# Kernel tuning notes

Hardware: AMD Instinct MI355X
Metric: run time of the kernel (lower is better)

The kernel has to match this reference:

```python
import jax, jax.numpy as jnp
import numpy as np

B, V = 4, 5                      # batch_size, nview
CUBE = (80, 80, 20)              # PICT_STRUCT.CUBE_SIZE
NBINS = CUBE[0] * CUBE[1] * CUBE[2]
IMG_W, IMG_H = 960, 512          # NETWORK.IMAGE_SIZE (w, h)
ORI_W, ORI_H = 1920, 1080        # NETWORK.ORI_IMAGE_SIZE
HM_W, HM_H = 240, 128            # NETWORK.HEATMAP_SIZE
C_IMG, C_FEAT = 3, 32
C_TOT = C_IMG + C_FEAT
HID = 256
D_IN = 3 + 2 * C_TOT             # points + [mean, var] volume features


def setup_inputs():
    key = jax.random.key(0)
    ks = jax.random.split(key, 10)
    denorm_imgs = jax.random.uniform(ks[0], (V, B, C_IMG, IMG_H, IMG_W), jnp.float32)
    feats2d = jax.random.normal(ks[1], (V, B, C_FEAT, HM_H, HM_W), jnp.float32)
    lo = jnp.array([-1500.0, -1500.0, -300.0], jnp.float32)
    hi = jnp.array([1500.0, 1500.0, 300.0], jnp.float32)
    grids = lo + (hi - lo) * jax.random.uniform(ks[2], (B, NBINS, 3), jnp.float32)
    # near-identity rotations, camera centers ~3m behind the volume so all
    # points project inside the original image
    R = jnp.tile(jnp.eye(3, dtype=jnp.float32), (V, B, 1, 1)) \
        + 0.01 * jax.random.normal(ks[3], (V, B, 3, 3), jnp.float32)
    T = jnp.tile(jnp.array([0.0, 0.0, -3000.0], jnp.float32).reshape(3, 1), (V, B, 1, 1)) \
        + 50.0 * jax.random.normal(ks[4], (V, B, 3, 1), jnp.float32)
    f = 1500.0 + 10.0 * jax.random.normal(ks[5], (V, B, 2), jnp.float32)
    c_cam = jnp.tile(jnp.array([ORI_W / 2.0, ORI_H / 2.0], jnp.float32), (V, B, 1))
    k_dist = jnp.zeros((V, B, 3), jnp.float32)
    p_dist = jnp.zeros((V, B, 2), jnp.float32)
    resize_transform = jnp.array([[IMG_W / ORI_W, 0.0, 0.0],
                                  [0.0, IMG_H / ORI_H, 0.0]], jnp.float32)
    s1, s2 = 1.0 / np.sqrt(D_IN), 1.0 / np.sqrt(HID)
    W1 = (s1 * jax.random.normal(ks[6], (D_IN, HID))).astype(jnp.float32)
    b1 = jnp.zeros((HID,), jnp.float32)
    W2 = (s2 * jax.random.normal(ks[7], (HID, HID))).astype(jnp.float32)
    b2 = jnp.zeros((HID,), jnp.float32)
    W3 = (s2 * jax.random.normal(ks[8], (HID, 1))).astype(jnp.float32)
    b3 = jnp.zeros((1,), jnp.float32)
    return dict(denorm_imgs=denorm_imgs, feats2d=feats2d, grids=grids, R=R, T=T,
                f=f, c_cam=c_cam, k_dist=k_dist, p_dist=p_dist,
                resize_transform=resize_transform,
                W1=W1, b1=b1, W2=W2, b2=b2, W3=W3, b3=b3)


def _project(x, R, T, f, c, k, p):
    # voxelpose project_point_radial: x [N,3] world-mm -> [N,2] pixel coords
    xcam = R @ (x.T - T)                               # [3,N]
    y = xcam[:2] / (xcam[2:3] + 1e-5)                  # [2,N]
    r2 = jnp.sum(y * y, axis=0)
    radial = 1.0 + k[0] * r2 + k[1] * r2 ** 2 + k[2] * r2 ** 3
    tan = p[0] * y[1] + p[1] * y[0]
    y = y * (radial + 2.0 * tan)[None, :] + jnp.stack([p[1], p[0]])[:, None] * r2[None, :]
    return (f[:, None] * y + c[:, None]).T             # [N,2]


def _bilinear(img, gx, gy):
    # F.grid_sample bilinear, align_corners=True, padding_mode='zeros'
    # img: [C,H,W]; gx,gy: [N] in [-1,1] -> [C,N]
    C, H, W = img.shape
    x = (gx + 1.0) * 0.5 * (W - 1)
    y = (gy + 1.0) * 0.5 * (H - 1)
    x0, y0 = jnp.floor(x), jnp.floor(y)
    wx1, wy1 = x - x0, y - y0
    wx0, wy0 = 1.0 - wx1, 1.0 - wy1

    def tap(xi, yi):
        valid = (xi >= 0) & (xi <= W - 1) & (yi >= 0) & (yi <= H - 1)
        xi_c = jnp.clip(xi.astype(jnp.int32), 0, W - 1)
        yi_c = jnp.clip(yi.astype(jnp.int32), 0, H - 1)
        return img[:, yi_c, xi_c] * valid.astype(img.dtype)

    return (tap(x0, y0) * (wx0 * wy0) + tap(x0 + 1.0, y0) * (wx1 * wy0)
            + tap(x0, y0 + 1.0) * (wx0 * wy1) + tap(x0 + 1.0, y0 + 1.0) * (wx1 * wy1))


def _sample_view(img, feat, pts, R, T, f, c, k, p, trans):
    xy = _project(pts, R, T, f, c, k, p)
    xy = jnp.clip(xy, -1.0, float(max(ORI_W, ORI_H)))
    xy = jnp.concatenate([xy, jnp.ones((xy.shape[0], 1), xy.dtype)], axis=1) @ trans.T
    g = xy / jnp.array([IMG_W - 1.0, IMG_H - 1.0], jnp.float32) * 2.0 - 1.0
    si = _bilinear(img, g[:, 0], g[:, 1])              # [C_IMG, N]
    sf = _bilinear(feat, g[:, 0], g[:, 1])             # [C_FEAT, N]
    return jnp.concatenate([si, sf], axis=0)           # [C_TOT, N]


def reference(denorm_imgs, feats2d, grids, R, T, f, c_cam, k_dist, p_dist,
              resize_transform, W1, b1, W2, b2, W3, b3):
    per_b = jax.vmap(_sample_view, in_axes=(0, 0, 0, 0, 0, 0, 0, 0, 0, None))
    per_vb = jax.vmap(per_b, in_axes=(0, 0, None, 0, 0, 0, 0, 0, 0, None))
    cubes = per_vb(denorm_imgs, feats2d, grids, R, T, f, c_cam, k_dist, p_dist,
                   resize_transform)                   # [V,B,C,N]
    cubes = jnp.transpose(cubes, (1, 2, 3, 0))         # [B,C,N,V]
    mean = jnp.mean(cubes, axis=-1)                    # sum(cubes/nview)
    var = jnp.sum((cubes - mean[..., None]) ** 2, axis=-1) / V
    var = jnp.exp(-var)
    gvol = jnp.concatenate([mean, var], axis=1)        # [B,2C,N]
    # nerf_model.query_density: MLP over (points, per-point global volume feats)
    feat = jnp.concatenate([grids / 1000.0, jnp.swapaxes(gvol, 1, 2)], axis=-1)  # [B,N,D_IN]
    h = jax.nn.relu(feat @ W1 + b1)
    h = jax.nn.relu(h @ W2 + b2)
    density = jax.nn.softplus(h @ W3 + b3)             # [B,N,1]
    alpha = 1.0 - jnp.exp(-density)
    return alpha.reshape(B, 1, CUBE[0], CUBE[1], CUBE[2])
```

## Files before the change

### kernel.cpp

```cpp
#include <hip/hip_runtime.h>

#define NVIEW 5
#define BATCH 4
#define NPTS 128000
#define CIMG 3
#define CFEAT 32
#define CTOT 35
#define DIN 73
#define HID 256
#define IMG_W 960
#define IMG_H 512
#define HM_W 240
#define HM_H 128
#define HW_IMG (IMG_W * IMG_H)
#define HW_HM (HM_W * HM_H)

#define BP 32

#define NB_IMG  (NVIEW * BATCH * HW_IMG / 4 / 256)
#define NB_FEAT (NVIEW * BATCH * HW_HM / 256)
#define NB_W    44

typedef __attribute__((ext_vector_type(8))) short bf16x8;
typedef __attribute__((ext_vector_type(4))) float f32x4;
typedef __attribute__((ext_vector_type(4))) unsigned short ushort4v;
typedef __attribute__((ext_vector_type(8))) unsigned short ushort8v;

__device__ inline unsigned short bf16_rtne(float f) {
    unsigned u = __builtin_bit_cast(unsigned, f);
    u += 0x7FFFu + ((u >> 16) & 1u);
    return (unsigned short)(u >> 16);
}
__device__ inline float bf2f(unsigned short u) {
    return __builtin_bit_cast(float, ((unsigned)u) << 16);
}

struct Tap {
    int o00, o01, o10, o11;
    float w00, w01, w10, w11;
};

__device__ inline void make_tap(float gx, float gy, int W, int H, Tap& t) {
    float x = (gx + 1.0f) * 0.5f * (float)(W - 1);
    float y = (gy + 1.0f) * 0.5f * (float)(H - 1);
    float x0 = floorf(x), y0 = floorf(y);
    float x1 = x0 + 1.0f, y1 = y0 + 1.0f;
    float wx1 = x - x0, wy1 = y - y0;
    float wx0 = 1.0f - wx1, wy0 = 1.0f - wy1;
    float vx0 = (x0 >= 0.0f && x0 <= (float)(W - 1)) ? 1.0f : 0.0f;
    float vx1 = (x1 >= 0.0f && x1 <= (float)(W - 1)) ? 1.0f : 0.0f;
    float vy0 = (y0 >= 0.0f && y0 <= (float)(H - 1)) ? 1.0f : 0.0f;
    float vy1 = (y1 >= 0.0f && y1 <= (float)(H - 1)) ? 1.0f : 0.0f;
    int ix0 = min(max((int)x0, 0), W - 1);
    int ix1 = min(max((int)x1, 0), W - 1);
    int iy0 = min(max((int)y0, 0), H - 1);
    int iy1 = min(max((int)y1, 0), H - 1);
    t.o00 = iy0 * W + ix0;  t.w00 = wx0 * wy0 * vx0 * vy0;
    t.o01 = iy0 * W + ix1;  t.w01 = wx1 * wy0 * vx1 * vy0;
    t.o10 = iy1 * W + ix0;  t.w10 = wx0 * wy1 * vx0 * vy1;
    t.o11 = iy1 * W + ix1;  t.w11 = wx1 * wy1 * vx1 * vy1;
}

__device__ inline float4 f4zero() { float4 r; r.x = r.y = r.z = r.w = 0.f; return r; }
__device__ inline float4 tapacc(ushort4v a, float w, float4 acc) {
    acc.x += w * bf2f(a[0]); acc.y += w * bf2f(a[1]);
    acc.z += w * bf2f(a[2]); acc.w += w * bf2f(a[3]); return acc;
}
__device__ inline float4 f4add(float4 a, float4 b) {
    a.x += b.x; a.y += b.y; a.z += b.z; a.w += b.w; return a;
}
__device__ inline float4 f4addsq(float4 acc, float4 v) {
    acc.x += v.x * v.x; acc.y += v.y * v.y; acc.z += v.z * v.z; acc.w += v.w * v.w; return acc;
}

__global__ __launch_bounds__(256) void prep_all(const float* __restrict__ imgs,
                                                const float* __restrict__ feats,
                                                const float* __restrict__ W1,
                                                const float* __restrict__ W2,
                                                unsigned short* __restrict__ wsImg,
                                                unsigned short* __restrict__ wsFeat,
                                                unsigned short* __restrict__ W1b,
                                                unsigned short* __restrict__ W2b) {
    int blk = blockIdx.x;
    if (blk < NB_IMG) {
        int idx = blk * 256 + threadIdx.x;
        int vb = idx / (HW_IMG / 4);
        int p4 = idx - vb * (HW_IMG / 4);
        const float* src = imgs + (size_t)vb * 3 * HW_IMG + p4 * 4;
        float4 c0 = *reinterpret_cast<const float4*>(src);
        float4 c1 = *reinterpret_cast<const float4*>(src + HW_IMG);
        float4 c2 = *reinterpret_cast<const float4*>(src + 2 * HW_IMG);
        ushort8v o01, o23;
        o01[0] = bf16_rtne(c0.x); o01[1] = bf16_rtne(c1.x); o01[2] = bf16_rtne(c2.x); o01[3] = 0;
        o01[4] = bf16_rtne(c0.y); o01[5] = bf16_rtne(c1.y); o01[6] = bf16_rtne(c2.y); o01[7] = 0;
        o23[0] = bf16_rtne(c0.z); o23[1] = bf16_rtne(c1.z); o23[2] = bf16_rtne(c2.z); o23[3] = 0;
        o23[4] = bf16_rtne(c0.w); o23[5] = bf16_rtne(c1.w); o23[6] = bf16_rtne(c2.w); o23[7] = 0;
        ushort8v* dst = reinterpret_cast<ushort8v*>(wsImg + ((size_t)vb * HW_IMG + p4 * 4) * 4);
        dst[0] = o01;
        dst[1] = o23;
    } else if (blk < NB_IMG + NB_FEAT) {
        int idx = (blk - NB_IMG) * 256 + threadIdx.x;
        int vb = idx / HW_HM;
        int pix = idx - vb * HW_HM;
        const float* src = feats + (size_t)vb * 32 * HW_HM + pix;
        ushort8v* dst = reinterpret_cast<ushort8v*>(wsFeat + (size_t)idx * 32);
#pragma unroll
        for (int k = 0; k < 4; ++k) {
            ushort8v o;
#pragma unroll
            for (int j = 0; j < 8; ++j)
                o[j] = bf16_rtne(src[(8 * k + j) * HW_HM]);
            dst[k] = o;
        }
    } else {
        int idx = (blk - NB_IMG - NB_FEAT) * 256 + threadIdx.x;
        if (idx < 16 * 3 * 64) {
            int l = idx & 63;
            int ks = (idx >> 6) % 3;
            int nt = idx / 192;
            int n = nt * 16 + (l & 15);
            int k0 = ks * 32 + (l >> 4) * 8;
            ushort8v o;
#pragma unroll
            for (int j = 0; j < 8; ++j) {
                int k = k0 + j;
                float v = (k < DIN) ? W1[k * HID + n] : 0.0f;
                o[j] = bf16_rtne(v);
            }
            reinterpret_cast<ushort8v*>(W1b)[idx] = o;
        } else if (idx < 16 * 3 * 64 + 16 * 8 * 64) {
            int id2 = idx - 16 * 3 * 64;
            int l = id2 & 63;
            int ks = (id2 >> 6) & 7;
            int nt = id2 >> 9;
            int n = nt * 16 + (l & 15);
            int k0 = ks * 32 + (l >> 4) * 8;
            ushort8v o;
#pragma unroll
            for (int j = 0; j < 8; ++j)
                o[j] = bf16_rtne(W2[(k0 + j) * HID + n]);
            reinterpret_cast<ushort8v*>(W2b)[id2] = o;
        }
    }
}

__global__ __launch_bounds__(256, 6) void fused_denorm_project(
    const unsigned short* __restrict__ wsImg,
    const unsigned short* __restrict__ wsFeat,
    const unsigned short* __restrict__ W1b,
    const unsigned short* __restrict__ W2b,
    const float* __restrict__ grids,
    const float* __restrict__ Rm,
    const float* __restrict__ Tm,
    const float* __restrict__ fcam,
    const float* __restrict__ ccam,
    const float* __restrict__ kdist,
    const float* __restrict__ pdist,
    const float* __restrict__ trans,
    const float* __restrict__ b1,
    const float* __restrict__ b2,
    const float* __restrict__ W3,
    const float* __restrict__ b3,
    float* __restrict__ out)
{
    __shared__ unsigned short featb[BP * 96];
    __shared__ unsigned short h1T[BP * 256];
    __shared__ float b1L[HID], b2L[HID], w3L[HID];
    __shared__ float partial[4][BP];

    const int tid = threadIdx.x;
    const int blk = blockIdx.x;
    const int b   = blk / (NPTS / BP);
    const int n0  = (blk % (NPTS / BP)) * BP;

    b1L[tid] = b1[tid];
    b2L[tid] = b2[tid];
    w3L[tid] = W3[tid];

    {
        const int t = tid & 7;
        const int p = tid >> 3;
        const int n = n0 + p;
        char* fbB = (char*)featb;
        const int rowoff = p * 192;
        const int sw = (p & 7) << 4;

        const float px = grids[(b * NPTS + n) * 3 + 0];
        const float py = grids[(b * NPTS + n) * 3 + 1];
        const float pz = grids[(b * NPTS + n) * 3 + 2];
        if (t == 1) {
            *(unsigned short*)(fbB + ((rowoff + 0) ^ sw)) = bf16_rtne(px * 1e-3f);
            *(unsigned short*)(fbB + ((rowoff + 2) ^ sw)) = bf16_rtne(py * 1e-3f);
            *(unsigned short*)(fbB + ((rowoff + 4) ^ sw)) = bf16_rtne(pz * 1e-3f);
        }
        {
            int c0 = 73 + t * 3;
            int cnt = (t == 7) ? 2 : 3;
            for (int j = 0; j < cnt; ++j)
                *(unsigned short*)(fbB + ((rowoff + (c0 + j) * 2) ^ sw)) = 0;
        }

        Tap myF = {}; Tap myI = {};
        if (t < NVIEW) {
            const int vb = t * BATCH + b;
            const float* Rp = Rm + vb * 9;
            const float* Tp = Tm + vb * 3;
            float X = px - Tp[0], Y = py - Tp[1], Z = pz - Tp[2];
            float xc = Rp[0] * X + Rp[1] * Y + Rp[2] * Z;
            float yc = Rp[3] * X + Rp[4] * Y + Rp[5] * Z;
            float zc = Rp[6] * X + Rp[7] * Y + Rp[8] * Z;
            float inv = 1.0f / (zc + 1e-5f);
            float y0 = xc * inv, y1 = yc * inv;
            float r2 = y0 * y0 + y1 * y1;
            float k0 = kdist[vb * 3 + 0], k1 = kdist[vb * 3 + 1], k2 = kdist[vb * 3 + 2];
            float p0 = pdist[vb * 2 + 0], p1 = pdist[vb * 2 + 1];
            float radial = 1.0f + r2 * (k0 + r2 * (k1 + r2 * k2));
            float tn = p0 * y1 + p1 * y0;
            float scl = radial + 2.0f * tn;
            float uu = y0 * scl + p1 * r2;
            float vv = y1 * scl + p0 * r2;
            float xo = fcam[vb * 2 + 0] * uu + ccam[vb * 2 + 0];
            float yo = fcam[vb * 2 + 1] * vv + ccam[vb * 2 + 1];
            xo = fminf(fmaxf(xo, -1.0f), 1920.0f);
            yo = fminf(fmaxf(yo, -1.0f), 1920.0f);
            float xr = trans[0] * xo + trans[1] * yo + trans[2];
            float yr = trans[3] * xo + trans[4] * yo + trans[5];
            float gx = xr * (1.0f / (float)(IMG_W - 1)) * 2.0f - 1.0f;
            float gy = yr * (1.0f / (float)(IMG_H - 1)) * 2.0f - 1.0f;
            make_tap(gx, gy, HM_W, HM_H, myF);
            make_tap(gx, gy, IMG_W, IMG_H, myI);
        }

        float4 s4 = f4zero(), q4 = f4zero();
        const int lb = (tid & 63) & 56;
        for (int v = 0; v < NVIEW; ++v) {
            const int src = lb + v;
            Tap tF;
            tF.o00 = __shfl(myF.o00, src, 64);
            tF.o01 = __shfl(myF.o01, src, 64);
            tF.o10 = __shfl(myF.o10, src, 64);
            tF.o11 = __shfl(myF.o11, src, 64);
            tF.w00 = __shfl(myF.w00, src, 64);
            tF.w01 = __shfl(myF.w01, src, 64);
            tF.w10 = __shfl(myF.w10, src, 64);
            tF.w11 = __shfl(myF.w11, src, 64);
            const unsigned short* fb = wsFeat + (size_t)(v * BATCH + b) * HW_HM * 32 + t * 4;
            ushort4v a00 = *reinterpret_cast<const ushort4v*>(fb + (size_t)tF.o00 * 32);
            ushort4v a01 = *reinterpret_cast<const ushort4v*>(fb + (size_t)tF.o01 * 32);
            ushort4v a10 = *reinterpret_cast<const ushort4v*>(fb + (size_t)tF.o10 * 32);
            ushort4v a11 = *reinterpret_cast<const ushort4v*>(fb + (size_t)tF.o11 * 32);
            float4 val = f4zero();
            val = tapacc(a00, tF.w00, val);
            val = tapacc(a01, tF.w01, val);
            val = tapacc(a10, tF.w10, val);
            val = tapacc(a11, tF.w11, val);
            s4 = f4add(s4, val);
            q4 = f4addsq(q4, val);
        }

        float4 si = f4zero(), qi = f4zero();
        if (t < NVIEW) {
            const unsigned short* ib = wsImg + (size_t)(t * BATCH + b) * HW_IMG * 4;
            ushort4v i00 = *reinterpret_cast<const ushort4v*>(ib + (size_t)myI.o00 * 4);
            ushort4v i01 = *reinterpret_cast<const ushort4v*>(ib + (size_t)myI.o01 * 4);
            ushort4v i10 = *reinterpret_cast<const ushort4v*>(ib + (size_t)myI.o10 * 4);
            ushort4v i11 = *reinterpret_cast<const ushort4v*>(ib + (size_t)myI.o11 * 4);
            float4 vi = f4zero();
            vi = tapacc(i00, myI.w00, vi);
            vi = tapacc(i01, myI.w01, vi);
            vi = tapacc(i10, myI.w10, vi);
            vi = tapacc(i11, myI.w11, vi);
            si = vi;
            qi = f4addsq(f4zero(), vi);
        }
#pragma unroll
        for (int off = 1; off <= 4; off <<= 1) {
            si.x += __shfl_xor(si.x, off, 64);
            si.y += __shfl_xor(si.y, off, 64);
            si.z += __shfl_xor(si.z, off, 64);
            qi.x += __shfl_xor(qi.x, off, 64);
            qi.y += __shfl_xor(qi.y, off, 64);
            qi.z += __shfl_xor(qi.z, off, 64);
        }

        const float inv5 = 1.0f / (float)NVIEW;
        {
            float m0 = s4.x * inv5, m1 = s4.y * inv5, m2 = s4.z * inv5, m3 = s4.w * inv5;
            int cm = 6 + 4 * t;
            int cv = 41 + 4 * t;
            *(unsigned short*)(fbB + ((rowoff + (cm + 0) * 2) ^ sw)) = bf16_rtne(m0);
            *(unsigned short*)(fbB + ((rowoff + (cm + 1) * 2) ^ sw)) = bf16_rtne(m1);
            *(unsigned short*)(fbB + ((rowoff + (cm + 2) * 2) ^ sw)) = bf16_rtne(m2);
            *(unsigned short*)(fbB + ((rowoff + (cm + 3) * 2) ^ sw)) = bf16_rtne(m3);
            *(unsigned short*)(fbB + ((rowoff + (cv + 0) * 2) ^ sw)) = bf16_rtne(expf(-(q4.x * inv5 - m0 * m0)));
            *(unsigned short*)(fbB + ((rowoff + (cv + 1) * 2) ^ sw)) = bf16_rtne(expf(-(q4.y * inv5 - m1 * m1)));
            *(unsigned short*)(fbB + ((rowoff + (cv + 2) * 2) ^ sw)) = bf16_rtne(expf(-(q4.z * inv5 - m2 * m2)));
            *(unsigned short*)(fbB + ((rowoff + (cv + 3) * 2) ^ sw)) = bf16_rtne(expf(-(q4.w * inv5 - m3 * m3)));
        }
        if (t == 0) {
            float m0 = si.x * inv5, m1 = si.y * inv5, m2 = si.z * inv5;
            *(unsigned short*)(fbB + ((rowoff + 3 * 2) ^ sw)) = bf16_rtne(m0);
            *(unsigned short*)(fbB + ((rowoff + 4 * 2) ^ sw)) = bf16_rtne(m1);
            *(unsigned short*)(fbB + ((rowoff + 5 * 2) ^ sw)) = bf16_rtne(m2);
            *(unsigned short*)(fbB + ((rowoff + 38 * 2) ^ sw)) = bf16_rtne(expf(-(qi.x * inv5 - m0 * m0)));
            *(unsigned short*)(fbB + ((rowoff + 39 * 2) ^ sw)) = bf16_rtne(expf(-(qi.y * inv5 - m1 * m1)));
            *(unsigned short*)(fbB + ((rowoff + 40 * 2) ^ sw)) = bf16_rtne(expf(-(qi.z * inv5 - m2 * m2)));
        }
    }
    __syncthreads();

    const int l   = tid & 63;
    const int w   = tid >> 6;
    const int g   = l >> 4;
    const int c16 = l & 15;

    {
        f32x4 acc[4][2];
#pragma unroll
        for (int nl = 0; nl < 4; ++nl)
#pragma unroll
            for (int pt = 0; pt < 2; ++pt) acc[nl][pt] = (f32x4)0.0f;

        const bf16x8* wfrag = reinterpret_cast<const bf16x8*>(W1b);
#pragma unroll
        for (int ks = 0; ks < 3; ++ks) {
            bf16x8 bfr[2];
#pragma unroll
            for (int pt = 0; pt < 2; ++pt) {
                int p = pt * 16 + c16;
                int off = (p * 192 + (ks * 32 + g * 8) * 2) ^ ((p & 7) << 4);
                bfr[pt] = *reinterpret_cast<const bf16x8*>((const char*)featb + off);
            }
#pragma unroll
            for (int nl = 0; nl < 4; ++nl) {
                int nt = w * 4 + nl;
                bf16x8 a = wfrag[(nt * 3 + ks) * 64 + l];
                acc[nl][0] = __builtin_amdgcn_mfma_f32_16x16x32_bf16(a, bfr[0], acc[nl][0], 0, 0, 0);
                acc[nl][1] = __builtin_amdgcn_mfma_f32_16x16x32_bf16(a, bfr[1], acc[nl][1], 0, 0, 0);
            }
        }
#pragma unroll
        for (int nl = 0; nl < 4; ++nl) {
            int nb = (w * 4 + nl) * 16 + g * 4;
            float bb0 = b1L[nb + 0], bb1 = b1L[nb + 1], bb2 = b1L[nb + 2], bb3v = b1L[nb + 3];
#pragma unroll
            for (int pt = 0; pt < 2; ++pt) {
                int p = pt * 16 + c16;
                ushort4v pk;
                pk[0] = bf16_rtne(fmaxf(acc[nl][pt][0] + bb0, 0.0f));
                pk[1] = bf16_rtne(fmaxf(acc[nl][pt][1] + bb1, 0.0f));
                pk[2] = bf16_rtne(fmaxf(acc[nl][pt][2] + bb2, 0.0f));
                pk[3] = bf16_rtne(fmaxf(acc[nl][pt][3] + bb3v, 0.0f));
                int off = (p * 512 + nb * 2) ^ ((p & 7) << 4);
                *reinterpret_cast<ushort4v*>((char*)h1T + off) = pk;
            }
        }
    }
    __syncthreads();

    {
        f32x4 acc[4][2];
#pragma unroll
        for (int nl = 0; nl < 4; ++nl)
#pragma unroll
            for (int pt = 0; pt < 2; ++pt) acc[nl][pt] = (f32x4)0.0f;

        const bf16x8* wfrag = reinterpret_cast<const bf16x8*>(W2b);
#pragma unroll
        for (int ks = 0; ks < 8; ++ks) {
            bf16x8 bfr[2];
#pragma unroll
            for (int pt = 0; pt < 2; ++pt) {
                int p = pt * 16 + c16;
                int off = (p * 512 + (ks * 32 + g * 8) * 2) ^ ((p & 7) << 4);
                bfr[pt] = *reinterpret_cast<const bf16x8*>((const char*)h1T + off);
            }
#pragma unroll
            for (int nl = 0; nl < 4; ++nl) {
                int nt = w * 4 + nl;
                bf16x8 a = wfrag[(nt * 8 + ks) * 64 + l];
                acc[nl][0] = __builtin_amdgcn_mfma_f32_16x16x32_bf16(a, bfr[0], acc[nl][0], 0, 0, 0);
                acc[nl][1] = __builtin_amdgcn_mfma_f32_16x16x32_bf16(a, bfr[1], acc[nl][1], 0, 0, 0);
            }
        }
        float s0 = 0.0f, s1 = 0.0f;
#pragma unroll
        for (int nl = 0; nl < 4; ++nl) {
            int nb = (w * 4 + nl) * 16 + g * 4;
#pragma unroll
            for (int r = 0; r < 4; ++r) {
                float b2v = b2L[nb + r];
                float w3v = w3L[nb + r];
                s0 += fmaxf(acc[nl][0][r] + b2v, 0.0f) * w3v;
                s1 += fmaxf(acc[nl][1][r] + b2v, 0.0f) * w3v;
            }
        }
        s0 += __shfl_xor(s0, 16, 64);
        s0 += __shfl_xor(s0, 32, 64);
        s1 += __shfl_xor(s1, 16, 64);
        s1 += __shfl_xor(s1, 32, 64);
        if (g == 0) {
            partial[w][c16]      = s0;
            partial[w][16 + c16] = s1;
        }
    }
    __syncthreads();

    if (tid < BP) {
        float v = partial[0][tid] + partial[1][tid] + partial[2][tid] + partial[3][tid] + b3[0];
        out[b * NPTS + n0 + tid] = 1.0f / (1.0f + expf(-v));
    }
}

extern "C" void kernel_launch(void* const* d_in, const int* in_sizes, int n_in,
                              void* d_out, int out_size, void* d_ws, size_t ws_size,
                              hipStream_t stream) {
    const float* imgs  = (const float*)d_in[0];
    const float* feats = (const float*)d_in[1];
    const float* grids = (const float*)d_in[2];
    const float* Rm    = (const float*)d_in[3];
    const float* Tm    = (const float*)d_in[4];
    const float* fcam  = (const float*)d_in[5];
    const float* ccam  = (const float*)d_in[6];
    const float* kdist = (const float*)d_in[7];
    const float* pdist = (const float*)d_in[8];
    const float* trans = (const float*)d_in[9];
    const float* W1    = (const float*)d_in[10];
    const float* b1    = (const float*)d_in[11];
    const float* W2    = (const float*)d_in[12];
    const float* b2    = (const float*)d_in[13];
    const float* W3    = (const float*)d_in[14];
    const float* b3    = (const float*)d_in[15];
    float* out = (float*)d_out;

    unsigned short* wsImg  = (unsigned short*)d_ws;
    unsigned short* wsFeat = wsImg + (size_t)NVIEW * BATCH * HW_IMG * 4;
    unsigned short* W1b    = wsFeat + (size_t)NVIEW * BATCH * HW_HM * 32;
    unsigned short* W2b    = W1b + 16 * 3 * 64 * 8;

    prep_all<<<NB_IMG + NB_FEAT + NB_W, 256, 0, stream>>>(
        imgs, feats, W1, W2, wsImg, wsFeat, W1b, W2b);

    const int nblocks = BATCH * (NPTS / BP);
    fused_denorm_project<<<nblocks, 256, 0, stream>>>(
        wsImg, wsFeat, W1b, W2b, grids, Rm, Tm, fcam, ccam, kdist, pdist, trans,
        b1, b2, W3, b3, out);
}
```

Measured before the change: 490.4 us.

## Merge prep and main kernels into one persistent kernel with grid barrier

Replaces the separate bf16 conversion kernel and the per-tile MLP kernel with a single persistent kernel of fixed grid size. Each block first runs grid-stride conversion of images, features and weights, then all blocks meet at an atomic-counter grid barrier, then each block loops over point tiles. This removes one kernel launch and the gap between the two kernels, and lets blocks stay resident across tiles. It adds a memset per call and relies on all 1536 blocks being co-resident, otherwise the spin barrier deadlocks. It also drops the tail overlap the launch boundary previously allowed.

```diff
diff --git a/kernel.cpp b/kernel.cpp
--- a/kernel.cpp
+++ b/kernel.cpp
@@ -16,10 +16,8 @@
 #define HW_HM (HM_W * HM_H)
 
 #define BP 32
-
-#define NB_IMG  (NVIEW * BATCH * HW_IMG / 4 / 256)
-#define NB_FEAT (NVIEW * BATCH * HW_HM / 256)
-#define NB_W    44
+#define TILES (BATCH * (NPTS / BP))
+#define GRID 1536
 
 typedef __attribute__((ext_vector_type(8))) short bf16x8;
 typedef __attribute__((ext_vector_type(4))) float f32x4;
@@ -73,19 +71,35 @@
     acc.x += v.x * v.x; acc.y += v.y * v.y; acc.z += v.z * v.z; acc.w += v.w * v.w; return acc;
 }
 
-__global__ __launch_bounds__(256) void prep_all(const float* __restrict__ imgs,
-                                                const float* __restrict__ feats,
-                                                const float* __restrict__ W1,
-                                                const float* __restrict__ W2,
-                                                unsigned short* __restrict__ wsImg,
-                                                unsigned short* __restrict__ wsFeat,
-                                                unsigned short* __restrict__ W1b,
-                                                unsigned short* __restrict__ W2b) {
-    int blk = blockIdx.x;
-    if (blk < NB_IMG) {
-        int idx = blk * 256 + threadIdx.x;
-        int vb = idx / (HW_IMG / 4);
-        int p4 = idx - vb * (HW_IMG / 4);
+__global__ __launch_bounds__(256, 6) void fused_all(
+    const float* __restrict__ imgs,
+    const float* __restrict__ feats,
+    const float* __restrict__ grids,
+    const float* __restrict__ Rm, const float* __restrict__ Tm,
+    const float* __restrict__ fcam, const float* __restrict__ ccam,
+    const float* __restrict__ kdist, const float* __restrict__ pdist,
+    const float* __restrict__ trans,
+    const float* __restrict__ W1, const float* __restrict__ b1,
+    const float* __restrict__ W2, const float* __restrict__ b2,
+    const float* __restrict__ W3, const float* __restrict__ b3,
+    unsigned short* __restrict__ wsImg,
+    unsigned short* __restrict__ wsFeat,
+    unsigned short* __restrict__ W1b,
+    unsigned short* __restrict__ W2b,
+    unsigned* __restrict__ ctr,
+    float* __restrict__ out)
+{
+    __shared__ unsigned short featb[BP * 96];
+    __shared__ unsigned short h1T[BP * 256];
+    __shared__ float b1L[HID], b2L[HID], w3L[HID];
+    __shared__ float partial[4][BP];
+
+    const int tid = threadIdx.x;
+    const unsigned gtid = blockIdx.x * 256u + (unsigned)tid;
+
+    for (unsigned u = gtid; u < (unsigned)(NVIEW * BATCH) * (HW_IMG / 4); u += GRID * 256u) {
+        unsigned vb = u / (HW_IMG / 4);
+        unsigned p4 = u - vb * (HW_IMG / 4);
         const float* src = imgs + (size_t)vb * 3 * HW_IMG + p4 * 4;
         float4 c0 = *reinterpret_cast<const float4*>(src);
         float4 c1 = *reinterpret_cast<const float4*>(src + HW_IMG);
@@ -98,12 +112,12 @@
         ushort8v* dst = reinterpret_cast<ushort8v*>(wsImg + ((size_t)vb * HW_IMG + p4 * 4) * 4);
         dst[0] = o01;
         dst[1] = o23;
-    } else if (blk < NB_IMG + NB_FEAT) {
-        int idx = (blk - NB_IMG) * 256 + threadIdx.x;
-        int vb = idx / HW_HM;
-        int pix = idx - vb * HW_HM;
+    }
+    for (unsigned u = gtid; u < (unsigned)(NVIEW * BATCH) * HW_HM; u += GRID * 256u) {
+        unsigned vb = u / HW_HM;
+        unsigned pix = u - vb * HW_HM;
         const float* src = feats + (size_t)vb * 32 * HW_HM + pix;
-        ushort8v* dst = reinterpret_cast<ushort8v*>(wsFeat + (size_t)idx * 32);
+        ushort8v* dst = reinterpret_cast<ushort8v*>(wsFeat + (size_t)u * 32);
 #pragma unroll
         for (int k = 0; k < 4; ++k) {
             ushort8v o;
@@ -112,303 +126,289 @@
                 o[j] = bf16_rtne(src[(8 * k + j) * HW_HM]);
             dst[k] = o;
         }
-    } else {
-        int idx = (blk - NB_IMG - NB_FEAT) * 256 + threadIdx.x;
-        if (idx < 16 * 3 * 64) {
-            int l = idx & 63;
-            int ks = (idx >> 6) % 3;
-            int nt = idx / 192;
-            int n = nt * 16 + (l & 15);
-            int k0 = ks * 32 + (l >> 4) * 8;
-            ushort8v o;
-#pragma unroll
-            for (int j = 0; j < 8; ++j) {
-                int k = k0 + j;
-                float v = (k < DIN) ? W1[k * HID + n] : 0.0f;
-                o[j] = bf16_rtne(v);
-            }
-            reinterpret_cast<ushort8v*>(W1b)[idx] = o;
-        } else if (idx < 16 * 3 * 64 + 16 * 8 * 64) {
-            int id2 = idx - 16 * 3 * 64;
-            int l = id2 & 63;
-            int ks = (id2 >> 6) & 7;
-            int nt = id2 >> 9;
-            int n = nt * 16 + (l & 15);
-            int k0 = ks * 32 + (l >> 4) * 8;
-            ushort8v o;
-#pragma unroll
-            for (int j = 0; j < 8; ++j)
-                o[j] = bf16_rtne(W2[(k0 + j) * HID + n]);
-            reinterpret_cast<ushort8v*>(W2b)[id2] = o;
-        }
     }
-}
-
-__global__ __launch_bounds__(256, 6) void fused_denorm_project(
-    const unsigned short* __restrict__ wsImg,
-    const unsigned short* __restrict__ wsFeat,
-    const unsigned short* __restrict__ W1b,
-    const unsigned short* __restrict__ W2b,
-    const float* __restrict__ grids,
-    const float* __restrict__ Rm,
-    const float* __restrict__ Tm,
-    const float* __restrict__ fcam,
-    const float* __restrict__ ccam,
-    const float* __restrict__ kdist,
-    const float* __restrict__ pdist,
-    const float* __restrict__ trans,
-    const float* __restrict__ b1,
-    const float* __restrict__ b2,
-    const float* __restrict__ W3,
-    const float* __restrict__ b3,
-    float* __restrict__ out)
-{
-    __shared__ unsigned short featb[BP * 96];
-    __shared__ unsigned short h1T[BP * 256];
-    __shared__ float b1L[HID], b2L[HID], w3L[HID];
-    __shared__ float partial[4][BP];
-
-    const int tid = threadIdx.x;
-    const int blk = blockIdx.x;
-    const int b   = blk / (NPTS / BP);
-    const int n0  = (blk % (NPTS / BP)) * BP;
+    if (gtid < 16 * 3 * 64) {
+        int idx = (int)gtid;
+        int l = idx & 63;
+        int ks = (idx >> 6) % 3;
+        int nt = idx / 192;
+        int n = nt * 16 + (l & 15);
+        int k0 = ks * 32 + (l >> 4) * 8;
+        ushort8v o;
+#pragma unroll
+        for (int j = 0; j < 8; ++j) {
+            int k = k0 + j;
+            float v = (k < DIN) ? W1[k * HID + n] : 0.0f;
+            o[j] = bf16_rtne(v);
+        }
+        reinterpret_cast<ushort8v*>(W1b)[idx] = o;
+    } else if (gtid < 16 * 3 * 64 + 16 * 8 * 64) {
+        int id2 = (int)gtid - 16 * 3 * 64;
+        int l = id2 & 63;
+        int ks = (id2 >> 6) & 7;
+        int nt = id2 >> 9;
+        int n = nt * 16 + (l & 15);
+        int k0 = ks * 32 + (l >> 4) * 8;
+        ushort8v o;
+#pragma unroll
+        for (int j = 0; j < 8; ++j)
+            o[j] = bf16_rtne(W2[(k0 + j) * HID + n]);
+        reinterpret_cast<ushort8v*>(W2b)[id2] = o;
+    }
+
+    __syncthreads();
+    if (tid == 0) {
+        __hip_atomic_fetch_add(ctr, 1u, __ATOMIC_RELEASE, __HIP_MEMORY_SCOPE_AGENT);
+        while (__hip_atomic_load(ctr, __ATOMIC_RELAXED, __HIP_MEMORY_SCOPE_AGENT) < (unsigned)GRID)
+            __builtin_amdgcn_s_sleep(8);
+        (void)__hip_atomic_load(ctr, __ATOMIC_ACQUIRE, __HIP_MEMORY_SCOPE_AGENT);
+    }
+    __syncthreads();
 
     b1L[tid] = b1[tid];
     b2L[tid] = b2[tid];
     w3L[tid] = W3[tid];
 
-    {
-        const int t = tid & 7;
-        const int p = tid >> 3;
-        const int n = n0 + p;
-        char* fbB = (char*)featb;
-        const int rowoff = p * 192;
-        const int sw = (p & 7) << 4;
-
-        const float px = grids[(b * NPTS + n) * 3 + 0];
-        const float py = grids[(b * NPTS + n) * 3 + 1];
-        const float pz = grids[(b * NPTS + n) * 3 + 2];
-        if (t == 1) {
-            *(unsigned short*)(fbB + ((rowoff + 0) ^ sw)) = bf16_rtne(px * 1e-3f);
-            *(unsigned short*)(fbB + ((rowoff + 2) ^ sw)) = bf16_rtne(py * 1e-3f);
-            *(unsigned short*)(fbB + ((rowoff + 4) ^ sw)) = bf16_rtne(pz * 1e-3f);
-        }
+    const float t00 = trans[0], t01 = trans[1], t02 = trans[2];
+    const float t10 = trans[3], t11 = trans[4], t12 = trans[5];
+
+    for (int tile = blockIdx.x; tile < TILES; tile += GRID) {
+        const int b  = tile / (NPTS / BP);
+        const int n0 = (tile % (NPTS / BP)) * BP;
+
         {
-            int c0 = 73 + t * 3;
-            int cnt = (t == 7) ? 2 : 3;
-            for (int j = 0; j < cnt; ++j)
-                *(unsigned short*)(fbB + ((rowoff + (c0 + j) * 2) ^ sw)) = 0;
-        }
-
-        Tap myF = {}; Tap myI = {};
-        if (t < NVIEW) {
-            const int vb = t * BATCH + b;
-            const float* Rp = Rm + vb * 9;
-            const float* Tp = Tm + vb * 3;
-            float X = px - Tp[0], Y = py - Tp[1], Z = pz - Tp[2];
-            float xc = Rp[0] * X + Rp[1] * Y + Rp[2] * Z;
-            float yc = Rp[3] * X + Rp[4] * Y + Rp[5] * Z;
-            float zc = Rp[6] * X + Rp[7] * Y + Rp[8] * Z;
-            float inv = 1.0f / (zc + 1e-5f);
-            float y0 = xc * inv, y1 = yc * inv;
-            float r2 = y0 * y0 + y1 * y1;
-            float k0 = kdist[vb * 3 + 0], k1 = kdist[vb * 3 + 1], k2 = kdist[vb * 3 + 2];
-            float p0 = pdist[vb * 2 + 0], p1 = pdist[vb * 2 + 1];
-            float radial = 1.0f + r2 * (k0 + r2 * (k1 + r2 * k2));
-            float tn = p0 * y1 + p1 * y0;
-            float scl = radial + 2.0f * tn;
-            float uu = y0 * scl + p1 * r2;
-            float vv = y1 * scl + p0 * r2;
-            float xo = fcam[vb * 2 + 0] * uu + ccam[vb * 2 + 0];
-            float yo = fcam[vb * 2 + 1] * vv + ccam[vb * 2 + 1];
-            xo = fminf(fmaxf(xo, -1.0f), 1920.0f);
-            yo = fminf(fmaxf(yo, -1.0f), 1920.0f);
-            float xr = trans[0] * xo + trans[1] * yo + trans[2];
-            float yr = trans[3] * xo + trans[4] * yo + trans[5];
-            float gx = xr * (1.0f / (float)(IMG_W - 1)) * 2.0f - 1.0f;
-            float gy = yr * (1.0f / (float)(IMG_H - 1)) * 2.0f - 1.0f;
-            make_tap(gx, gy, HM_W, HM_H, myF);
-            make_tap(gx, gy, IMG_W, IMG_H, myI);
-        }
-
-        float4 s4 = f4zero(), q4 = f4zero();
-        const int lb = (tid & 63) & 56;
-        for (int v = 0; v < NVIEW; ++v) {
-            const int src = lb + v;
-            Tap tF;
-            tF.o00 = __shfl(myF.o00, src, 64);
-            tF.o01 = __shfl(myF.o01, src, 64);
-            tF.o10 = __shfl(myF.o10, src, 64);
-            tF.o11 = __shfl(myF.o11, src, 64);
-            tF.w00 = __shfl(myF.w00, src, 64);
-            tF.w01 = __shfl(myF.w01, src, 64);
-            tF.w10 = __shfl(myF.w10, src, 64);
-            tF.w11 = __shfl(myF.w11, src, 64);
-            const unsigned short* fb = wsFeat + (size_t)(v * BATCH + b) * HW_HM * 32 + t * 4;
-            ushort4v a00 = *reinterpret_cast<const ushort4v*>(fb + (size_t)tF.o00 * 32);
-            ushort4v a01 = *reinterpret_cast<const ushort4v*>(fb + (size_t)tF.o01 * 32);
-            ushort4v a10 = *reinterpret_cast<const ushort4v*>(fb + (size_t)tF.o10 * 32);
-            ushort4v a11 = *reinterpret_cast<const ushort4v*>(fb + (size_t)tF.o11 * 32);
-            float4 val = f4zero();
-            val = tapacc(a00, tF.w00, val);
-            val = tapacc(a01, tF.w01, val);
-            val = tapacc(a10, tF.w10, val);
-            val = tapacc(a11, tF.w11, val);
-            s4 = f4add(s4, val);
-            q4 = f4addsq(q4, val);
-        }
-
-        float4 si = f4zero(), qi = f4zero();
-        if (t < NVIEW) {
-            const unsigned short* ib = wsImg + (size_t)(t * BATCH + b) * HW_IMG * 4;
-            ushort4v i00 = *reinterpret_cast<const ushort4v*>(ib + (size_t)myI.o00 * 4);
-            ushort4v i01 = *reinterpret_cast<const ushort4v*>(ib + (size_t)myI.o01 * 4);
-            ushort4v i10 = *reinterpret_cast<const ushort4v*>(ib + (size_t)myI.o10 * 4);
-            ushort4v i11 = *reinterpret_cast<const ushort4v*>(ib + (size_t)myI.o11 * 4);
-            float4 vi = f4zero();
-            vi = tapacc(i00, myI.w00, vi);
-            vi = tapacc(i01, myI.w01, vi);
-            vi = tapacc(i10, myI.w10, vi);
-            vi = tapacc(i11, myI.w11, vi);
-            si = vi;
-            qi = f4addsq(f4zero(), vi);
-        }
-#pragma unroll
-        for (int off = 1; off <= 4; off <<= 1) {
-            si.x += __shfl_xor(si.x, off, 64);
-            si.y += __shfl_xor(si.y, off, 64);
-            si.z += __shfl_xor(si.z, off, 64);
-            qi.x += __shfl_xor(qi.x, off, 64);
-            qi.y += __shfl_xor(qi.y, off, 64);
-            qi.z += __shfl_xor(qi.z, off, 64);
-        }
-
-        const float inv5 = 1.0f / (float)NVIEW;
+            const int t = tid & 7;
+            const int p = tid >> 3;
+            const int n = n0 + p;
+            char* fbB = (char*)featb;
+            const int rowoff = p * 192;
+            const int sw = (p & 7) << 4;
+
+            const float px = grids[(b * NPTS + n) * 3 + 0];
+            const float py = grids[(b * NPTS + n) * 3 + 1];
+            const float pz = grids[(b * NPTS + n) * 3 + 2];
+            if (t == 1) {
+                *(unsigned short*)(fbB + ((rowoff + 0) ^ sw)) = bf16_rtne(px * 1e-3f);
+                *(unsigned short*)(fbB + ((rowoff + 2) ^ sw)) = bf16_rtne(py * 1e-3f);
+                *(unsigned short*)(fbB + ((rowoff + 4) ^ sw)) = bf16_rtne(pz * 1e-3f);
+            }
+            {
+                int c0 = 73 + t * 3;
+                int cnt = (t == 7) ? 2 : 3;
+                for (int j = 0; j < cnt; ++j)
+                    *(unsigned short*)(fbB + ((rowoff + (c0 + j) * 2) ^ sw)) = 0;
+            }
+
+            Tap myF = {}; Tap myI = {};
+            if (t < NVIEW) {
+                const int vb = t * BATCH + b;
+                const float* Rp = Rm + vb * 9;
+                const float* Tp = Tm + vb * 3;
+                float X = px - Tp[0], Y = py - Tp[1], Z = pz - Tp[2];
+                float xc = Rp[0] * X + Rp[1] * Y + Rp[2] * Z;
+                float yc = Rp[3] * X + Rp[4] * Y + Rp[5] * Z;
+                float zc = Rp[6] * X + Rp[7] * Y + Rp[8] * Z;
+                float inv = 1.0f / (zc + 1e-5f);
+                float y0 = xc * inv, y1 = yc * inv;
+                float r2 = y0 * y0 + y1 * y1;
+                float k0 = kdist[vb * 3 + 0], k1 = kdist[vb * 3 + 1], k2 = kdist[vb * 3 + 2];
+                float p0 = pdist[vb * 2 + 0], p1 = pdist[vb * 2 + 1];
+                float radial = 1.0f + r2 * (k0 + r2 * (k1 + r2 * k2));
+                float tn = p0 * y1 + p1 * y0;
+                float scl = radial + 2.0f * tn;
+                float uu = y0 * scl + p1 * r2;
+                float vv = y1 * scl + p0 * r2;
+                float xo = fcam[vb * 2 + 0] * uu + ccam[vb * 2 + 0];
+                float yo = fcam[vb * 2 + 1] * vv + ccam[vb * 2 + 1];
+                xo = fminf(fmaxf(xo, -1.0f), 1920.0f);
+                yo = fminf(fmaxf(yo, -1.0f), 1920.0f);
+                float xr = t00 * xo + t01 * yo + t02;
+                float yr = t10 * xo + t11 * yo + t12;
+                float gx = xr * (1.0f / (float)(IMG_W - 1)) * 2.0f - 1.0f;
+                float gy = yr * (1.0f / (float)(IMG_H - 1)) * 2.0f - 1.0f;
+                make_tap(gx, gy, HM_W, HM_H, myF);
+                make_tap(gx, gy, IMG_W, IMG_H, myI);
+            }
+
+            float4 s4 = f4zero(), q4 = f4zero();
+            const int lb = (tid & 63) & 56;
+            for (int v = 0; v < NVIEW; ++v) {
+                const int src = lb + v;
+                Tap tF;
+                tF.o00 = __shfl(myF.o00, src, 64);
+                tF.o01 = __shfl(myF.o01, src, 64);
+                tF.o10 = __shfl(myF.o10, src, 64);
+                tF.o11 = __shfl(myF.o11, src, 64);
+                tF.w00 = __shfl(myF.w00, src, 64);
+                tF.w01 = __shfl(myF.w01, src, 64);
+                tF.w10 = __shfl(myF.w10, src, 64);
+                tF.w11 = __shfl(myF.w11, src, 64);
+                const unsigned short* fb = wsFeat + (size_t)(v * BATCH + b) * HW_HM * 32 + t * 4;
+                ushort4v a00 = *reinterpret_cast<const ushort4v*>(fb + (size_t)tF.o00 * 32);
+                ushort4v a01 = *reinterpret_cast<const ushort4v*>(fb + (size_t)tF.o01 * 32);
+                ushort4v a10 = *reinterpret_cast<const ushort4v*>(fb + (size_t)tF.o10 * 32);
+                ushort4v a11 = *reinterpret_cast<const ushort4v*>(fb + (size_t)tF.o11 * 32);
+                float4 val = f4zero();
+                val = tapacc(a00, tF.w00, val);
+                val = tapacc(a01, tF.w01, val);
+                val = tapacc(a10, tF.w10, val);
+                val = tapacc(a11, tF.w11, val);
+                s4 = f4add(s4, val);
+                q4 = f4addsq(q4, val);
+            }
+
+            float4 si = f4zero(), qi = f4zero();
+            if (t < NVIEW) {
+                const unsigned short* ib = wsImg + (size_t)(t * BATCH + b) * HW_IMG * 4;
+                ushort4v i00 = *reinterpret_cast<const ushort4v*>(ib + (size_t)myI.o00 * 4);
+                ushort4v i01 = *reinterpret_cast<const ushort4v*>(ib + (size_t)myI.o01 * 4);
+                ushort4v i10 = *reinterpret_cast<const ushort4v*>(ib + (size_t)myI.o10 * 4);
+                ushort4v i11 = *reinterpret_cast<const ushort4v*>(ib + (size_t)myI.o11 * 4);
+                float4 vi = f4zero();
+                vi = tapacc(i00, myI.w00, vi);
+                vi = tapacc(i01, myI.w01, vi);
+                vi = tapacc(i10, myI.w10, vi);
+                vi = tapacc(i11, myI.w11, vi);
+                si = vi;
+                qi = f4addsq(f4zero(), vi);
+            }
+#pragma unroll
+            for (int off = 1; off <= 4; off <<= 1) {
+                si.x += __shfl_xor(si.x, off, 64);
+                si.y += __shfl_xor(si.y, off, 64);
+                si.z += __shfl_xor(si.z, off, 64);
+                qi.x += __shfl_xor(qi.x, off, 64);
+                qi.y += __shfl_xor(qi.y, off, 64);
+                qi.z += __shfl_xor(qi.z, off, 64);
+            }
+
+            const float inv5 = 1.0f / (float)NVIEW;
+            {
+                float m0 = s4.x * inv5, m1 = s4.y * inv5, m2 = s4.z * inv5, m3 = s4.w * inv5;
+                int cm = 6 + 4 * t;
+                int cv = 41 + 4 * t;
+                *(unsigned short*)(fbB + ((rowoff + (cm + 0) * 2) ^ sw)) = bf16_rtne(m0);
+                *(unsigned short*)(fbB + ((rowoff + (cm + 1) * 2) ^ sw)) = bf16_rtne(m1);
+                *(unsigned short*)(fbB + ((rowoff + (cm + 2) * 2) ^ sw)) = bf16_rtne(m2);
+                *(unsigned short*)(fbB + ((rowoff + (cm + 3) * 2) ^ sw)) = bf16_rtne(m3);
+                *(unsigned short*)(fbB + ((rowoff + (cv + 0) * 2) ^ sw)) = bf16_rtne(expf(-(q4.x * inv5 - m0 * m0)));
+                *(unsigned short*)(fbB + ((rowoff + (cv + 1) * 2) ^ sw)) = bf16_rtne(expf(-(q4.y * inv5 - m1 * m1)));
+                *(unsigned short*)(fbB + ((rowoff + (cv + 2) * 2) ^ sw)) = bf16_rtne(expf(-(q4.z * inv5 - m2 * m2)));
+                *(unsigned short*)(fbB + ((rowoff + (cv + 3) * 2) ^ sw)) = bf16_rtne(expf(-(q4.w * inv5 - m3 * m3)));
+            }
+            if (t == 0) {
+                float m0 = si.x * inv5, m1 = si.y * inv5, m2 = si.z * inv5;
+                *(unsigned short*)(fbB + ((rowoff + 3 * 2) ^ sw)) = bf16_rtne(m0);
+                *(unsigned short*)(fbB + ((rowoff + 4 * 2) ^ sw)) = bf16_rtne(m1);
+                *(unsigned short*)(fbB + ((rowoff + 5 * 2) ^ sw)) = bf16_rtne(m2);
+                *(unsigned short*)(fbB + ((rowoff + 38 * 2) ^ sw)) = bf16_rtne(expf(-(qi.x * inv5 - m0 * m0)));
+                *(unsigned short*)(fbB + ((rowoff + 39 * 2) ^ sw)) = bf16_rtne(expf(-(qi.y * inv5 - m1 * m1)));
+                *(unsigned short*)(fbB + ((rowoff + 40 * 2) ^ sw)) = bf16_rtne(expf(-(qi.z * inv5 - m2 * m2)));
+            }
+        }
+        __syncthreads();
+
+        const int l   = tid & 63;
+        const int w   = tid >> 6;
+        const int g   = l >> 4;
+        const int c16 = l & 15;
+
         {
-            float m0 = s4.x * inv5, m1 = s4.y * inv5, m2 = s4.z * inv5, m3 = s4.w * inv5;
-            int cm = 6 + 4 * t;
-            int cv = 41 + 4 * t;
-            *(unsigned short*)(fbB + ((rowoff + (cm + 0) * 2) ^ sw)) = bf16_rtne(m0);
-            *(unsigned short*)(fbB + ((rowoff + (cm + 1) * 2) ^ sw)) = bf16_rtne(m1);
-            *(unsigned short*)(fbB + ((rowoff + (cm + 2) * 2) ^ sw)) = bf16_rtne(m2);
-            *(unsigned short*)(fbB + ((rowoff + (cm + 3) * 2) ^ sw)) = bf16_rtne(m3);
-            *(unsigned short*)(fbB + ((rowoff + (cv + 0) * 2) ^ sw)) = bf16_rtne(expf(-(q4.x * inv5 - m0 * m0)));
-            *(unsigned short*)(fbB + ((rowoff + (cv + 1) * 2) ^ sw)) = bf16_rtne(expf(-(q4.y * inv5 - m1 * m1)));
-            *(unsigned short*)(fbB + ((rowoff + (cv + 2) * 2) ^ sw)) = bf16_rtne(expf(-(q4.z * inv5 - m2 * m2)));
-            *(unsigned short*)(fbB + ((rowoff + (cv + 3) * 2) ^ sw)) = bf16_rtne(expf(-(q4.w * inv5 - m3 * m3)));
-        }
-        if (t == 0) {
-            float m0 = si.x * inv5, m1 = si.y * inv5, m2 = si.z * inv5;
-            *(unsigned short*)(fbB + ((rowoff + 3 * 2) ^ sw)) = bf16_rtne(m0);
-            *(unsigned short*)(fbB + ((rowoff + 4 * 2) ^ sw)) = bf16_rtne(m1);
-            *(unsigned short*)(fbB + ((rowoff + 5 * 2) ^ sw)) = bf16_rtne(m2);
-            *(unsigned short*)(fbB + ((rowoff + 38 * 2) ^ sw)) = bf16_rtne(expf(-(qi.x * inv5 - m0 * m0)));
-            *(unsigned short*)(fbB + ((rowoff + 39 * 2) ^ sw)) = bf16_rtne(expf(-(qi.y * inv5 - m1 * m1)));
-            *(unsigned short*)(fbB + ((rowoff + 40 * 2) ^ sw)) = bf16_rtne(expf(-(qi.z * inv5 - m2 * m2)));
-        }
-    }
-    __syncthreads();
-
-    const int l   = tid & 63;
-    const int w   = tid >> 6;
-    const int g   = l >> 4;
-    const int c16 = l & 15;
-
-    {
-        f32x4 acc[4][2];
-#pragma unroll
-        for (int nl = 0; nl < 4; ++nl)
-#pragma unroll
-            for (int pt = 0; pt < 2; ++pt) acc[nl][pt] = (f32x4)0.0f;
-
-        const bf16x8* wfrag = reinterpret_cast<const bf16x8*>(W1b);
-#pragma unroll
-        for (int ks = 0; ks < 3; ++ks) {
-            bf16x8 bfr[2];
-#pragma unroll
-            for (int pt = 0; pt < 2; ++pt) {
-                int p = pt * 16 + c16;
-                int off = (p * 192 + (ks * 32 + g * 8) * 2) ^ ((p & 7) << 4);
-                bfr[pt] = *reinterpret_cast<const bf16x8*>((const char*)featb + off);
+            f32x4 acc[4][2];
+#pragma unroll
+            for (int nl = 0; nl < 4; ++nl)
+#pragma unroll
+                for (int pt = 0; pt < 2; ++pt) acc[nl][pt] = (f32x4)0.0f;
+
+            const bf16x8* wfrag = reinterpret_cast<const bf16x8*>(W1b);
+#pragma unroll
+            for (int ks = 0; ks < 3; ++ks) {
+                bf16x8 bfr[2];
+#pragma unroll
+                for (int pt = 0; pt < 2; ++pt) {
+                    int p = pt * 16 + c16;
+                    int off = (p * 192 + (ks * 32 + g * 8) * 2) ^ ((p & 7) << 4);
+                    bfr[pt] = *reinterpret_cast<const bf16x8*>((const char*)featb + off);
+                }
+#pragma unroll
+                for (int nl = 0; nl < 4; ++nl) {
+                    int nt = w * 4 + nl;
+                    bf16x8 a = wfrag[(nt * 3 + ks) * 64 + l];
+                    acc[nl][0] = __builtin_amdgcn_mfma_f32_16x16x32_bf16(a, bfr[0], acc[nl][0], 0, 0, 0);
+                    acc[nl][1] = __builtin_amdgcn_mfma_f32_16x16x32_bf16(a, bfr[1], acc[nl][1], 0, 0, 0);
+                }
             }
 #pragma unroll
             for (int nl = 0; nl < 4; ++nl) {
-                int nt = w * 4 + nl;
-                bf16x8 a = wfrag[(nt * 3 + ks) * 64 + l];
-                acc[nl][0] = __builtin_amdgcn_mfma_f32_16x16x32_bf16(a, bfr[0], acc[nl][0], 0, 0, 0);
-                acc[nl][1] = __builtin_amdgcn_mfma_f32_16x16x32_bf16(a, bfr[1], acc[nl][1], 0, 0, 0);
-            }
-        }
-#pragma unroll
-        for (int nl = 0; nl < 4; ++nl) {
-            int nb = (w * 4 + nl) * 16 + g * 4;
-            float bb0 = b1L[nb + 0], bb1 = b1L[nb + 1], bb2 = b1L[nb + 2], bb3v = b1L[nb + 3];
-#pragma unroll
-            for (int pt = 0; pt < 2; ++pt) {
-                int p = pt * 16 + c16;
-                ushort4v pk;
-                pk[0] = bf16_rtne(fmaxf(acc[nl][pt][0] + bb0, 0.0f));
-                pk[1] = bf16_rtne(fmaxf(acc[nl][pt][1] + bb1, 0.0f));
-                pk[2] = bf16_rtne(fmaxf(acc[nl][pt][2] + bb2, 0.0f));
-                pk[3] = bf16_rtne(fmaxf(acc[nl][pt][3] + bb3v, 0.0f));
-                int off = (p * 512 + nb * 2) ^ ((p & 7) << 4);
-                *reinterpret_cast<ushort4v*>((char*)h1T + off) = pk;
-            }
-        }
-    }
-    __syncthreads();
-
-    {
-        f32x4 acc[4][2];
-#pragma unroll
-        for (int nl = 0; nl < 4; ++nl)
-#pragma unroll
-            for (int pt = 0; pt < 2; ++pt) acc[nl][pt] = (f32x4)0.0f;
-
-        const bf16x8* wfrag = reinterpret_cast<const bf16x8*>(W2b);
-#pragma unroll
-        for (int ks = 0; ks < 8; ++ks) {
-            bf16x8 bfr[2];
-#pragma unroll
-            for (int pt = 0; pt < 2; ++pt) {
-                int p = pt * 16 + c16;
-                int off = (p * 512 + (ks * 32 + g * 8) * 2) ^ ((p & 7) << 4);
-                bfr[pt] = *reinterpret_cast<const bf16x8*>((const char*)h1T + off);
-            }
+                int nb = (w * 4 + nl) * 16 + g * 4;
+                float bb0 = b1L[nb + 0], bb1 = b1L[nb + 1], bb2 = b1L[nb + 2], bb3v = b1L[nb + 3];
+#pragma unroll
+                for (int pt = 0; pt < 2; ++pt) {
+                    int p = pt * 16 + c16;
+                    ushort4v pk;
+                    pk[0] = bf16_rtne(fmaxf(acc[nl][pt][0] + bb0, 0.0f));
+                    pk[1] = bf16_rtne(fmaxf(acc[nl][pt][1] + bb1, 0.0f));
+                    pk[2] = bf16_rtne(fmaxf(acc[nl][pt][2] + bb2, 0.0f));
+                    pk[3] = bf16_rtne(fmaxf(acc[nl][pt][3] + bb3v, 0.0f));
+                    int off = (p * 512 + nb * 2) ^ ((p & 7) << 4);
+                    *reinterpret_cast<ushort4v*>((char*)h1T + off) = pk;
+                }
+            }
+        }
+        __syncthreads();
+
+        {
+            f32x4 acc[4][2];
+#pragma unroll
+            for (int nl = 0; nl < 4; ++nl)
+#pragma unroll
+                for (int pt = 0; pt < 2; ++pt) acc[nl][pt] = (f32x4)0.0f;
+
+            const bf16x8* wfrag = reinterpret_cast<const bf16x8*>(W2b);
+#pragma unroll
+            for (int ks = 0; ks < 8; ++ks) {
+                bf16x8 bfr[2];
+#pragma unroll
+                for (int pt = 0; pt < 2; ++pt) {
+                    int p = pt * 16 + c16;
+                    int off = (p * 512 + (ks * 32 + g * 8) * 2) ^ ((p & 7) << 4);
+                    bfr[pt] = *reinterpret_cast<const bf16x8*>((const char*)h1T + off);
+                }
+#pragma unroll
+                for (int nl = 0; nl < 4; ++nl) {
+                    int nt = w * 4 + nl;
+                    bf16x8 a = wfrag[(nt * 8 + ks) * 64 + l];
+                    acc[nl][0] = __builtin_amdgcn_mfma_f32_16x16x32_bf16(a, bfr[0], acc[nl][0], 0, 0, 0);
+                    acc[nl][1] = __builtin_amdgcn_mfma_f32_16x16x32_bf16(a, bfr[1], acc[nl][1], 0, 0, 0);
+                }
+            }
+            float s0 = 0.0f, s1 = 0.0f;
 #pragma unroll
             for (int nl = 0; nl < 4; ++nl) {
-                int nt = w * 4 + nl;
-                bf16x8 a = wfrag[(nt * 8 + ks) * 64 + l];
-                acc[nl][0] = __builtin_amdgcn_mfma_f32_16x16x32_bf16(a, bfr[0], acc[nl][0], 0, 0, 0);
-                acc[nl][1] = __builtin_amdgcn_mfma_f32_16x16x32_bf16(a, bfr[1], acc[nl][1], 0, 0, 0);
-            }
-        }
-        float s0 = 0.0f, s1 = 0.0f;
-#pragma unroll
-        for (int nl = 0; nl < 4; ++nl) {
-            int nb = (w * 4 + nl) * 16 + g * 4;
-#pragma unroll
-            for (int r = 0; r < 4; ++r) {
-                float b2v = b2L[nb + r];
-                float w3v = w3L[nb + r];
-                s0 += fmaxf(acc[nl][0][r] + b2v, 0.0f) * w3v;
-                s1 += fmaxf(acc[nl][1][r] + b2v, 0.0f) * w3v;
-            }
-        }
-        s0 += __shfl_xor(s0, 16, 64);
-        s0 += __shfl_xor(s0, 32, 64);
-        s1 += __shfl_xor(s1, 16, 64);
-        s1 += __shfl_xor(s1, 32, 64);
-        if (g == 0) {
-            partial[w][c16]      = s0;
-            partial[w][16 + c16] = s1;
-        }
-    }
-    __syncthreads();
-
-    if (tid < BP) {
-        float v = partial[0][tid] + partial[1][tid] + partial[2][tid] + partial[3][tid] + b3[0];
-        out[b * NPTS + n0 + tid] = 1.0f / (1.0f + expf(-v));
+                int nb = (w * 4 + nl) * 16 + g * 4;
+#pragma unroll
+                for (int r = 0; r < 4; ++r) {
+                    float b2v = b2L[nb + r];
+                    float w3v = w3L[nb + r];
+                    s0 += fmaxf(acc[nl][0][r] + b2v, 0.0f) * w3v;
+                    s1 += fmaxf(acc[nl][1][r] + b2v, 0.0f) * w3v;
+                }
+            }
+            s0 += __shfl_xor(s0, 16, 64);
+            s0 += __shfl_xor(s0, 32, 64);
+            s1 += __shfl_xor(s1, 16, 64);
+            s1 += __shfl_xor(s1, 32, 64);
+            if (g == 0) {
+                partial[w][c16]      = s0;
+                partial[w][16 + c16] = s1;
+            }
+        }
+        __syncthreads();
+
+        if (tid < BP) {
+            float v = partial[0][tid] + partial[1][tid] + partial[2][tid] + partial[3][tid] + b3[0];
+            out[b * NPTS + n0 + tid] = 1.0f / (1.0f + expf(-v));
+        }
     }
 }
 
@@ -437,12 +437,12 @@
     unsigned short* wsFeat = wsImg + (size_t)NVIEW * BATCH * HW_IMG * 4;
     unsigned short* W1b    = wsFeat + (size_t)NVIEW * BATCH * HW_HM * 32;
     unsigned short* W2b    = W1b + 16 * 3 * 64 * 8;
-
-    prep_all<<<NB_IMG + NB_FEAT + NB_W, 256, 0, stream>>>(
-        imgs, feats, W1, W2, wsImg, wsFeat, W1b, W2b);
-
-    const int nblocks = BATCH * (NPTS / BP);
-    fused_denorm_project<<<nblocks, 256, 0, stream>>>(
-        wsImg, wsFeat, W1b, W2b, grids, Rm, Tm, fcam, ccam, kdist, pdist, trans,
-        b1, b2, W3, b3, out);
-}
+    unsigned* ctr = (unsigned*)(W2b + 16 * 8 * 64 * 8);
+
+    hipMemsetAsync(ctr, 0, sizeof(unsigned), stream);
+
+    fused_all<<<GRID, 256, 0, stream>>>(
+        imgs, feats, grids, Rm, Tm, fcam, ccam, kdist, pdist, trans,
+        W1, b1, W2, b2, W3, b3,
+        wsImg, wsFeat, W1b, W2b, ctr, out);
+}
```

Measured after the change: 1.101 ms. 124% more time.
